# Optimization experiments

Measured on AMD Instinct MI355X. Metric: run time of the kernel, lower is better.

## Reference

```python
import jax, jax.numpy as jnp
import numpy as np

NUM_PT = 4
PATCH = 8
C = 33
HW = 256
HALF = PATCH // 2  # crop half-size = 4
NUM_HYPER = 16
NUM_PATCH = NUM_PT * 9  # 36
FEAT = C + NUM_PATCH * 2 + 2  # 33 + 72 + 2 = 107

# shift table exactly as in the torch module (note duplicated [0,8] entry)
SHIFTS = jnp.array([[-PATCH, 0], [-PATCH, PATCH], [0, PATCH], [PATCH, PATCH],
                    [PATCH, 0], [PATCH, -PATCH], [0, PATCH], [-PATCH, -PATCH],
                    [0, 0]], dtype=jnp.float32) / 255.0


def setup_inputs() -> dict:
    key = jax.random.key(0)
    ks = jax.random.split(key, 11)
    d = jax.random.normal(ks[0], (32, C, HW, HW), dtype=jnp.float32)
    x = jax.random.uniform(ks[1], (32, NUM_PT, 2), dtype=jnp.float32)
    conv_w = jax.random.normal(ks[2], (C, C, PATCH, PATCH), dtype=jnp.float32) * 0.02
    conv_b = jax.random.normal(ks[3], (C,), dtype=jnp.float32) * 0.02
    H = jax.random.normal(ks[4], (NUM_PATCH, NUM_HYPER), dtype=jnp.float32)
    T = jax.random.normal(ks[5], (NUM_PT, NUM_PATCH), dtype=jnp.float32)
    W = jnp.ones((1, NUM_HYPER), dtype=jnp.float32) / NUM_HYPER
    lin1_w = jax.random.normal(ks[6], (2, FEAT), dtype=jnp.float32) * 0.05
    lin1_b = jnp.zeros((2,), dtype=jnp.float32)
    lin2_w = jax.random.normal(ks[7], (9, FEAT), dtype=jnp.float32) * 0.05
    lin2_b = jnp.zeros((9,), dtype=jnp.float32)
    return dict(d=d, x=x, conv_w=conv_w, conv_b=conv_b, H=H, T=T, W=W,
                lin1_w=lin1_w, lin1_b=lin1_b, lin2_w=lin2_w, lin2_b=lin2_b)


def _crop_one(land, img_pad):
    # land: [2] normalized; img_pad: [C, HW+2*HALF, HW+2*HALF]
    # faithful to getcropedInputs: X=round(x*255), Y=round((y+1)*255), clip [0,255];
    # zero-padded 8x8 crop centered at (X, Y) == dynamic_slice on padded image at (X, Y)
    ix = jnp.clip(jnp.round(land[0] * (HW - 1)).astype(jnp.int32), 0, 255)
    iy = jnp.clip(jnp.round((land[1] + 1.0) * (HW - 1)).astype(jnp.int32), 0, 255)
    return jax.lax.dynamic_slice(img_pad, (0, ix, iy), (C, PATCH, PATCH))

_crop_batch = jax.vmap(_crop_one)  # over batch


def reference(d, x, conv_w, conv_b, H, T, W, lin1_w, lin1_b, lin2_w, lin2_b):
    b = d.shape[0]
    d_pad = jnp.pad(d, ((0, 0), (0, 0), (HALF, HALF), (HALF, HALF)))
    # --- get_hg_node_features (faithful to the i*j indexing + in-place shifts) ---
    lh = jnp.repeat(x, 9, axis=1)  # [b, 36, 2]
    crops = []
    for i in range(NUM_PT):
        for j in range(9):
            idx = i * j  # reproduces original indexing bug
            lh = lh.at[:, idx, :].add(SHIFTS[j])
            crops.append(_crop_batch(lh[:, idx, :], d_pad))  # [b, C, 8, 8]
    visual = jnp.stack(crops, axis=1)  # [b, 36, C, 8, 8]
    # valid 8x8 conv on 8x8 patch == full contraction per patch
    patch_feat = jnp.einsum('bnchw,ochw->bno', visual, conv_w) + conv_b  # [b,36,33]
    shape_feat = (lh[:, None, :, :] - lh[:, :, None, :]).reshape(b, NUM_PATCH, -1)  # [b,36,72]
    gin = jnp.concatenate([patch_feat, shape_feat, lh], axis=-1)  # [b,36,107]
    # --- ABHG hypergraph message passing ---
    M1 = (T @ (H * W[0])) @ H.T  # [4,36]
    message = jnp.einsum('pn,bnf->bpf', M1, gin)  # [b,4,107]
    k1, k2 = jax.random.split(jax.random.key(42))
    m1 = jax.random.bernoulli(k1, 0.9, message.shape).astype(message.dtype)
    m2 = jax.random.bernoulli(k2, 0.9, message.shape).astype(message.dtype)
    x1 = message * m1 / 0.9
    x2 = message * m2 / 0.9
    offset = jax.nn.sigmoid(x1 @ lin1_w.T + lin1_b)            # [b,4,2]
    direction = jax.nn.softmax(x2 @ lin2_w.T + lin2_b, axis=2)  # [b,4,9]
    shift = offset * (direction @ SHIFTS)                       # [b,4,2]
    updated = x + shift
    return updated * 255.0
```

## Files before the change

### kernel.cpp

```cpp
#include <hip/hip_runtime.h>
#include <math.h>

#ifndef JAX_PARTITIONABLE
#define JAX_PARTITIONABLE 1
#endif

#define NB 32
#define NC 33
#define HWDIM 256
#define NPATCH 36
#define FEAT 107
#define CROP_ELEMS 2112

__device__ __constant__ float c_SHX[9] = {
  -8.0f/255.0f, -8.0f/255.0f, 0.0f, 8.0f/255.0f, 8.0f/255.0f,
   8.0f/255.0f, 0.0f, -8.0f/255.0f, 0.0f };
__device__ __constant__ float c_SHY[9] = {
   0.0f, 8.0f/255.0f, 8.0f/255.0f, 8.0f/255.0f, 0.0f,
  -8.0f/255.0f, 8.0f/255.0f, -8.0f/255.0f, 0.0f };

__device__ inline void simulate_lh(const float* xb, float* clx, float* cly,
                                   float* lh ) {
  float lx[36], ly[36];
  for (int n = 0; n < 36; ++n) { lx[n] = xb[(n/9)*2]; ly[n] = xb[(n/9)*2+1]; }
  int c = 0;
  for (int i = 0; i < 4; ++i)
    for (int j = 0; j < 9; ++j) {
      int idx = i * j;
      lx[idx] += c_SHX[j];
      ly[idx] += c_SHY[j];
      clx[c] = lx[idx]; cly[c] = ly[idx]; ++c;
    }
  for (int n = 0; n < 36; ++n) { lh[n*2] = lx[n]; lh[n*2+1] = ly[n]; }
}

__global__ __launch_bounds__(256) void patch_feat_kernel(
    const float* __restrict__ d, const float* __restrict__ x,
    const float* __restrict__ conv_w, const float* __restrict__ conv_b,
    float* __restrict__ pf) {
  const int b = blockIdx.x;
  const int n = blockIdx.y;
  __shared__ float s_crop[CROP_ELEMS];
  __shared__ float s_land[2];
  if (threadIdx.x == 0) {
    float clx[36], cly[36], lh[72];
    simulate_lh(x + b * 8, clx, cly, lh);
    s_land[0] = clx[n]; s_land[1] = cly[n];
  }
  __syncthreads();
  const float lxv = s_land[0], lyv = s_land[1];
  int ix = (int)rintf(lxv * 255.0f);
  ix = ix < 0 ? 0 : (ix > 255 ? 255 : ix);
  int iy = (int)rintf((lyv + 1.0f) * 255.0f);
  iy = iy < 0 ? 0 : (iy > 255 ? 255 : iy);
  const float* db = d + (size_t)b * NC * HWDIM * HWDIM;
  for (int k = threadIdx.x; k < CROP_ELEMS; k += 256) {
    int c = k >> 6;
    int u = (k >> 3) & 7;
    int v = k & 7;
    int r = ix + u - 4;
    int col = iy + v - 4;
    float val = 0.0f;
    if (r >= 0 && r < HWDIM && col >= 0 && col < HWDIM)
      val = db[(c * HWDIM + r) * HWDIM + col];
    s_crop[k] = val;
  }
  __syncthreads();
  const int wave = threadIdx.x >> 6;
  const int lane = threadIdx.x & 63;
  for (int o = wave; o < NC; o += 4) {
    const float* w = conv_w + o * CROP_ELEMS;
    float acc = 0.0f;
    #pragma unroll
    for (int k = 0; k < 33; ++k) {
      int e = lane + (k << 6);
      acc += s_crop[e] * w[e];
    }
    #pragma unroll
    for (int off = 32; off > 0; off >>= 1)
      acc += __shfl_xor(acc, off, 64);
    if (lane == 0) pf[(b * NPATCH + n) * NC + o] = acc + conv_b[o];
  }
}

__device__ inline void tf2x32(unsigned k0, unsigned k1, unsigned x0, unsigned x1,
                              unsigned& o0, unsigned& o1) {
  unsigned ks2 = k0 ^ k1 ^ 0x1BD11BDAu;
#define TFR(r) { x0 += x1; x1 = (x1 << r) | (x1 >> (32 - r)); x1 ^= x0; }
  x0 += k0; x1 += k1;
  TFR(13) TFR(15) TFR(26) TFR(6)
  x0 += k1;  x1 += ks2 + 1u;
  TFR(17) TFR(29) TFR(16) TFR(24)
  x0 += ks2; x1 += k0 + 2u;
  TFR(13) TFR(15) TFR(26) TFR(6)
  x0 += k0;  x1 += k1 + 3u;
  TFR(17) TFR(29) TFR(16) TFR(24)
  x0 += k1;  x1 += ks2 + 4u;
  TFR(13) TFR(15) TFR(26) TFR(6)
  x0 += ks2; x1 += k0 + 5u;
#undef TFR
  o0 = x0; o1 = x1;
}

__device__ inline float drop_mask(unsigned ka, unsigned kb, unsigned idx) {
#if JAX_PARTITIONABLE
  unsigned b0, b1;
  tf2x32(ka, kb, 0u, idx, b0, b1);
  unsigned bits = b0 ^ b1;
#else
  const unsigned half = 6848u;
  unsigned ln = idx < half ? idx : idx - half;
  unsigned b0, b1;
  tf2x32(ka, kb, ln, ln + half, b0, b1);
  unsigned bits = idx < half ? b0 : b1;
#endif
  float u = __uint_as_float((bits >> 9) | 0x3F800000u) - 1.0f;
  return u < 0.9f ? 1.0f : 0.0f;
}

__global__ __launch_bounds__(64) void head_kernel(
    const float* __restrict__ x, const float* __restrict__ H,
    const float* __restrict__ T, const float* __restrict__ W,
    const float* __restrict__ lin1w, const float* __restrict__ lin1b,
    const float* __restrict__ lin2w, const float* __restrict__ lin2b,
    const float* __restrict__ pf, float* __restrict__ out) {
  const int b = blockIdx.x >> 2;
  const int p = blockIdx.x & 3;
  const int lane = threadIdx.x;
  __shared__ float s_lh[72];
  __shared__ float s_A[16];
  __shared__ float s_M1[36];
  if (lane == 0) {
    float clx[36], cly[36];
    simulate_lh(x + b * 8, clx, cly, s_lh);
  }
  __syncthreads();
  if (lane < 16) {
    float a = 0.0f;
    for (int k = 0; k < 36; ++k)
      a += T[p * 36 + k] * (H[k * 16 + lane] * W[lane]);
    s_A[lane] = a;
  }
  __syncthreads();
  if (lane < 36) {
    float m = 0.0f;
    for (int h = 0; h < 16; ++h) m += s_A[h] * H[lane * 16 + h];
    s_M1[lane] = m;
  }
  __syncthreads();

  const int f0 = lane;
  const int f1 = lane + 64;
  const bool has1 = (f1 < FEAT);
  float msg0 = 0.0f, msg1 = 0.0f;
  const float* pfb = pf + b * NPATCH * NC;
  for (int n = 0; n < 36; ++n) {
    float m1v = s_M1[n];
    float g0;
    if (f0 < 33) g0 = pfb[n * 33 + f0];
    else if (f0 < 105) {
      int q = f0 - 33; int mm = q >> 1, cc = q & 1;
      g0 = s_lh[mm * 2 + cc] - s_lh[n * 2 + cc];
    } else g0 = s_lh[n * 2 + (f0 - 105)];
    msg0 += m1v * g0;
    if (has1) {
      float g1;
      if (f1 < 105) {
        int q = f1 - 33; int mm = q >> 1, cc = q & 1;
        g1 = s_lh[mm * 2 + cc] - s_lh[n * 2 + cc];
      } else g1 = s_lh[n * 2 + (f1 - 105)];
      msg1 += m1v * g1;
    }
  }

  unsigned k1a, k1b, k2a, k2b;
#if JAX_PARTITIONABLE
  tf2x32(0u, 42u, 0u, 0u, k1a, k1b);
  tf2x32(0u, 42u, 0u, 1u, k2a, k2b);
#else
  { unsigned a0, c0, a1, c1;
    tf2x32(0u, 42u, 0u, 2u, a0, c0);
    tf2x32(0u, 42u, 1u, 3u, a1, c1);
    k1a = a0; k1b = a1; k2a = c0; k2b = c1; }
#endif
  unsigned base = (unsigned)((b * 4 + p) * FEAT);
  float x1_0 = msg0 * drop_mask(k1a, k1b, base + f0) / 0.9f;
  float x2_0 = msg0 * drop_mask(k2a, k2b, base + f0) / 0.9f;
  float x1_1 = 0.0f, x2_1 = 0.0f;
  if (has1) {
    x1_1 = msg1 * drop_mask(k1a, k1b, base + f1) / 0.9f;
    x2_1 = msg1 * drop_mask(k2a, k2b, base + f1) / 0.9f;
  }

  float r[11];
  #pragma unroll
  for (int k = 0; k < 2; ++k) {
    float v = x1_0 * lin1w[k * FEAT + f0];
    if (has1) v += x1_1 * lin1w[k * FEAT + f1];
    r[k] = v;
  }
  #pragma unroll
  for (int j = 0; j < 9; ++j) {
    float v = x2_0 * lin2w[j * FEAT + f0];
    if (has1) v += x2_1 * lin2w[j * FEAT + f1];
    r[2 + j] = v;
  }
  #pragma unroll
  for (int off = 32; off > 0; off >>= 1) {
    #pragma unroll
    for (int k = 0; k < 11; ++k) r[k] += __shfl_xor(r[k], off, 64);
  }
  if (lane == 0) {
    float o0 = 1.0f / (1.0f + expf(-(r[0] + lin1b[0])));
    float o1 = 1.0f / (1.0f + expf(-(r[1] + lin1b[1])));
    float lg[9], mx = -1e30f;
    for (int j = 0; j < 9; ++j) { lg[j] = r[2 + j] + lin2b[j]; if (lg[j] > mx) mx = lg[j]; }
    float s = 0.0f;
    for (int j = 0; j < 9; ++j) { lg[j] = expf(lg[j] - mx); s += lg[j]; }
    float sx = 0.0f, sy = 0.0f;
    for (int j = 0; j < 9; ++j) {
      float dj = lg[j] / s;
      sx += dj * c_SHX[j];
      sy += dj * c_SHY[j];
    }
    int o = (b * 4 + p) * 2;
    out[o + 0] = (x[b * 8 + p * 2 + 0] + o0 * sx) * 255.0f;
    out[o + 1] = (x[b * 8 + p * 2 + 1] + o1 * sy) * 255.0f;
  }
}

extern "C" void kernel_launch(void* const* d_in, const int* in_sizes, int n_in,
                              void* d_out, int out_size, void* d_ws, size_t ws_size,
                              hipStream_t stream) {
  const float* d     = (const float*)d_in[0];
  const float* x     = (const float*)d_in[1];
  const float* convw = (const float*)d_in[2];
  const float* convb = (const float*)d_in[3];
  const float* H     = (const float*)d_in[4];
  const float* T     = (const float*)d_in[5];
  const float* W     = (const float*)d_in[6];
  const float* l1w   = (const float*)d_in[7];
  const float* l1b   = (const float*)d_in[8];
  const float* l2w   = (const float*)d_in[9];
  const float* l2b   = (const float*)d_in[10];
  float* out = (float*)d_out;
  float* pf  = (float*)d_ws;

  dim3 g1(NB, NPATCH);
  patch_feat_kernel<<<g1, 256, 0, stream>>>(d, x, convw, convb, pf);
  head_kernel<<<NB * 4, 64, 0, stream>>>(x, H, T, W, l1w, l1b, l2w, l2b, pf, out);
}
```

Before: 370.5 us.

## Process two crops per block, reuse conv weights, precompute landmark shift tables

Each patch-feature block now handles two crops, so every conv weight loaded from global memory is reused across both crops. The crop values are held in registers as float4 and the output channels are split statically across waves. The serial single-thread landmark simulation is replaced by constexpr lookup tables, evaluated per thread in both kernels. The non-partitionable RNG path is removed. The cost is higher register pressure and half as many blocks in the grid.

```diff
diff --git a/kernel.cpp b/kernel.cpp
--- a/kernel.cpp
+++ b/kernel.cpp
@@ -1,9 +1,5 @@
 #include <hip/hip_runtime.h>
 #include <math.h>
-
-#ifndef JAX_PARTITIONABLE
-#define JAX_PARTITIONABLE 1
-#endif
 
 #define NB 32
 #define NC 33
@@ -11,6 +7,7 @@
 #define NPATCH 36
 #define FEAT 107
 #define CROP_ELEMS 2112
+#define CPB 2
 
 __device__ __constant__ float c_SHX[9] = {
   -8.0f/255.0f, -8.0f/255.0f, 0.0f, 8.0f/255.0f, 8.0f/255.0f,
@@ -19,67 +16,112 @@
    0.0f, 8.0f/255.0f, 8.0f/255.0f, 8.0f/255.0f, 0.0f,
   -8.0f/255.0f, 8.0f/255.0f, -8.0f/255.0f, 0.0f };
 
-__device__ inline void simulate_lh(const float* xb, float* clx, float* cly,
-                                   float* lh ) {
-  float lx[36], ly[36];
-  for (int n = 0; n < 36; ++n) { lx[n] = xb[(n/9)*2]; ly[n] = xb[(n/9)*2+1]; }
+struct Tables {
+  int pt[36];
+  int ch[36][12];
+  int ptS[36];
+  int chS[36][12];
+};
+constexpr Tables make_tables() {
+  Tables t = {};
+  int hits[36][12] = {};
+  int nh[36] = {};
   int c = 0;
   for (int i = 0; i < 4; ++i)
     for (int j = 0; j < 9; ++j) {
       int idx = i * j;
-      lx[idx] += c_SHX[j];
-      ly[idx] += c_SHY[j];
-      clx[c] = lx[idx]; cly[c] = ly[idx]; ++c;
-    }
-  for (int n = 0; n < 36; ++n) { lh[n*2] = lx[n]; lh[n*2+1] = ly[n]; }
-}
+      hits[idx][nh[idx]] = j; nh[idx]++;
+      t.pt[c] = idx / 9;
+      for (int k = 0; k < 12; ++k) t.ch[c][k] = (k < nh[idx]) ? hits[idx][k] : 8;
+      ++c;
+    }
+  for (int s = 0; s < 36; ++s) {
+    t.ptS[s] = s / 9;
+    for (int k = 0; k < 12; ++k) t.chS[s][k] = (k < nh[s]) ? hits[s][k] : 8;
+  }
+  return t;
+}
+__device__ __constant__ Tables c_tab = make_tables();
 
 __global__ __launch_bounds__(256) void patch_feat_kernel(
     const float* __restrict__ d, const float* __restrict__ x,
     const float* __restrict__ conv_w, const float* __restrict__ conv_b,
     float* __restrict__ pf) {
   const int b = blockIdx.x;
-  const int n = blockIdx.y;
-  __shared__ float s_crop[CROP_ELEMS];
-  __shared__ float s_land[2];
-  if (threadIdx.x == 0) {
-    float clx[36], cly[36], lh[72];
-    simulate_lh(x + b * 8, clx, cly, lh);
-    s_land[0] = clx[n]; s_land[1] = cly[n];
-  }
-  __syncthreads();
-  const float lxv = s_land[0], lyv = s_land[1];
-  int ix = (int)rintf(lxv * 255.0f);
-  ix = ix < 0 ? 0 : (ix > 255 ? 255 : ix);
-  int iy = (int)rintf((lyv + 1.0f) * 255.0f);
-  iy = iy < 0 ? 0 : (iy > 255 ? 255 : iy);
+  const int n0 = blockIdx.y * CPB;
+  __shared__ float s_crop[CPB][CROP_ELEMS];
+
   const float* db = d + (size_t)b * NC * HWDIM * HWDIM;
-  for (int k = threadIdx.x; k < CROP_ELEMS; k += 256) {
-    int c = k >> 6;
-    int u = (k >> 3) & 7;
-    int v = k & 7;
-    int r = ix + u - 4;
-    int col = iy + v - 4;
-    float val = 0.0f;
-    if (r >= 0 && r < HWDIM && col >= 0 && col < HWDIM)
-      val = db[(c * HWDIM + r) * HWDIM + col];
-    s_crop[k] = val;
-  }
-  __syncthreads();
+  #pragma unroll
+  for (int cc = 0; cc < CPB; ++cc) {
+    const int n = n0 + cc;
+    float lx = x[b * 8 + c_tab.pt[n] * 2 + 0];
+    float ly = x[b * 8 + c_tab.pt[n] * 2 + 1];
+    #pragma unroll
+    for (int t = 0; t < 12; ++t) {
+      int j = c_tab.ch[n][t];
+      lx += c_SHX[j]; ly += c_SHY[j];
+    }
+    int ix = (int)rintf(lx * 255.0f);
+    ix = ix < 0 ? 0 : (ix > 255 ? 255 : ix);
+    int iy = (int)rintf((ly + 1.0f) * 255.0f);
+    iy = iy < 0 ? 0 : (iy > 255 ? 255 : iy);
+    for (int k = threadIdx.x; k < CROP_ELEMS; k += 256) {
+      int c = k >> 6;
+      int u = (k >> 3) & 7;
+      int v = k & 7;
+      int r = ix + u - 4;
+      int col = iy + v - 4;
+      float val = 0.0f;
+      if (r >= 0 && r < HWDIM && col >= 0 && col < HWDIM)
+        val = db[(c * HWDIM + r) * HWDIM + col];
+      s_crop[cc][k] = val;
+    }
+  }
+  __syncthreads();
+
   const int wave = threadIdx.x >> 6;
   const int lane = threadIdx.x & 63;
-  for (int o = wave; o < NC; o += 4) {
+  float4 cr[CPB][8];
+  float ct[CPB];
+  #pragma unroll
+  for (int cc = 0; cc < CPB; ++cc) {
+    #pragma unroll
+    for (int k = 0; k < 8; ++k)
+      cr[cc][k] = *(const float4*)&s_crop[cc][k * 256 + lane * 4];
+    ct[cc] = s_crop[cc][2048 + lane];
+  }
+  const int obeg = (wave == 0) ? 0 : (9 + (wave - 1) * 8);
+  const int ocnt = (wave == 0) ? 9 : 8;
+  for (int oi = 0; oi < ocnt; ++oi) {
+    const int o = obeg + oi;
     const float* w = conv_w + o * CROP_ELEMS;
-    float acc = 0.0f;
-    #pragma unroll
-    for (int k = 0; k < 33; ++k) {
-      int e = lane + (k << 6);
-      acc += s_crop[e] * w[e];
-    }
-    #pragma unroll
-    for (int off = 32; off > 0; off >>= 1)
-      acc += __shfl_xor(acc, off, 64);
-    if (lane == 0) pf[(b * NPATCH + n) * NC + o] = acc + conv_b[o];
+    float acc[CPB];
+    #pragma unroll
+    for (int cc = 0; cc < CPB; ++cc) acc[cc] = 0.0f;
+    #pragma unroll
+    for (int k = 0; k < 8; ++k) {
+      float4 wv = *(const float4*)&w[k * 256 + lane * 4];
+      #pragma unroll
+      for (int cc = 0; cc < CPB; ++cc) {
+        acc[cc] += wv.x * cr[cc][k].x + wv.y * cr[cc][k].y +
+                   wv.z * cr[cc][k].z + wv.w * cr[cc][k].w;
+      }
+    }
+    float wt = w[2048 + lane];
+    #pragma unroll
+    for (int cc = 0; cc < CPB; ++cc) acc[cc] += wt * ct[cc];
+    #pragma unroll
+    for (int off = 32; off > 0; off >>= 1) {
+      #pragma unroll
+      for (int cc = 0; cc < CPB; ++cc)
+        acc[cc] += __shfl_xor(acc[cc], off, 64);
+    }
+    if (lane == 0) {
+      #pragma unroll
+      for (int cc = 0; cc < CPB; ++cc)
+        pf[(b * NPATCH + n0 + cc) * NC + o] = acc[cc] + conv_b[o];
+    }
   }
 }
 
@@ -103,17 +145,9 @@
 }
 
 __device__ inline float drop_mask(unsigned ka, unsigned kb, unsigned idx) {
-#if JAX_PARTITIONABLE
   unsigned b0, b1;
   tf2x32(ka, kb, 0u, idx, b0, b1);
   unsigned bits = b0 ^ b1;
-#else
-  const unsigned half = 6848u;
-  unsigned ln = idx < half ? idx : idx - half;
-  unsigned b0, b1;
-  tf2x32(ka, kb, ln, ln + half, b0, b1);
-  unsigned bits = idx < half ? b0 : b1;
-#endif
   float u = __uint_as_float((bits >> 9) | 0x3F800000u) - 1.0f;
   return u < 0.9f ? 1.0f : 0.0f;
 }
@@ -130,9 +164,16 @@
   __shared__ float s_lh[72];
   __shared__ float s_A[16];
   __shared__ float s_M1[36];
-  if (lane == 0) {
-    float clx[36], cly[36];
-    simulate_lh(x + b * 8, clx, cly, s_lh);
+  if (lane < 36) {
+    float vx = x[b * 8 + c_tab.ptS[lane] * 2 + 0];
+    float vy = x[b * 8 + c_tab.ptS[lane] * 2 + 1];
+    #pragma unroll
+    for (int t = 0; t < 12; ++t) {
+      int j = c_tab.chS[lane][t];
+      vx += c_SHX[j]; vy += c_SHY[j];
+    }
+    s_lh[lane * 2 + 0] = vx;
+    s_lh[lane * 2 + 1] = vy;
   }
   __syncthreads();
   if (lane < 16) {
@@ -174,15 +215,8 @@
   }
 
   unsigned k1a, k1b, k2a, k2b;
-#if JAX_PARTITIONABLE
   tf2x32(0u, 42u, 0u, 0u, k1a, k1b);
   tf2x32(0u, 42u, 0u, 1u, k2a, k2b);
-#else
-  { unsigned a0, c0, a1, c1;
-    tf2x32(0u, 42u, 0u, 2u, a0, c0);
-    tf2x32(0u, 42u, 1u, 3u, a1, c1);
-    k1a = a0; k1b = a1; k2a = c0; k2b = c1; }
-#endif
   unsigned base = (unsigned)((b * 4 + p) * FEAT);
   float x1_0 = msg0 * drop_mask(k1a, k1b, base + f0) / 0.9f;
   float x2_0 = msg0 * drop_mask(k2a, k2b, base + f0) / 0.9f;
@@ -246,7 +280,7 @@
   float* out = (float*)d_out;
   float* pf  = (float*)d_ws;
 
-  dim3 g1(NB, NPATCH);
+  dim3 g1(NB, NPATCH / CPB);
   patch_feat_kernel<<<g1, 256, 0, stream>>>(d, x, convw, convb, pf);
   head_kernel<<<NB * 4, 64, 0, stream>>>(x, H, T, W, l1w, l1b, l2w, l2b, pf, out);
 }
```

After: 356.8 us. 3.7% less time.
